# Kernel tuning notes

Measured on AMD Instinct MI355X. Metric: run time of the kernel, lower is better.

Reference implementation:

```python
import jax, jax.numpy as jnp
import numpy as np

N = 100000
E = 1600000
IN_C, HID_C, OUT_C = 128, 128, 64


def setup_inputs() -> dict:
    key = jax.random.key(0)
    k_x, k_e, k_w1, k_w2 = jax.random.split(key, 4)
    x = jax.random.normal(k_x, (N, IN_C), dtype=jnp.float32)
    edge_index = jax.random.randint(k_e, (2, E), 0, N, dtype=jnp.int32)
    # nn.Linear default init: U(-1/sqrt(fan_in), 1/sqrt(fan_in)); bias init zeros per module
    lim1 = 1.0 / np.sqrt(IN_C)
    lim2 = 1.0 / np.sqrt(HID_C)
    W1 = jax.random.uniform(k_w1, (IN_C, HID_C), minval=-lim1, maxval=lim1, dtype=jnp.float32)
    b1 = jnp.zeros((HID_C,), dtype=jnp.float32)
    W2 = jax.random.uniform(k_w2, (HID_C, OUT_C), minval=-lim2, maxval=lim2, dtype=jnp.float32)
    b2 = jnp.zeros((OUT_C,), dtype=jnp.float32)
    return {"x": x, "edge_index": edge_index, "W1": W1, "b1": b1, "W2": W2, "b2": b2}


def _out_degree_gcn_conv(x, src, dst, W, b, n_nodes):
    # linear projection (no bias in lin)
    h = x @ W  # [N, out_c]
    # out-degree of each source node
    deg = jax.ops.segment_sum(jnp.ones((src.shape[0],), dtype=h.dtype), src, num_segments=n_nodes)
    deg_inv = 1.0 / jnp.maximum(deg, 1.0)  # clamp(min=1)
    h = h * deg_inv[:, None]
    # message: x_j = h[src]; aggregate: sum at dst
    out = jax.ops.segment_sum(h[src], dst, num_segments=n_nodes)  # [N, out_c]
    return out + b


def reference(x, edge_index, W1, b1, W2, b2):
    src, dst = edge_index[0], edge_index[1]
    n = x.shape[0]
    h = _out_degree_gcn_conv(x, src, dst, W1, b1, n)
    h = jax.nn.relu(h)
    # dropout p=0.0 -> identity
    out = _out_degree_gcn_conv(h, src, dst, W2, b2, n)
    return out
```

## Files before the change

kernel.cpp:

```cpp
#include <hip/hip_runtime.h>
#include <hip/hip_bf16.h>


typedef __attribute__((ext_vector_type(8))) short short8;
typedef __attribute__((ext_vector_type(4))) float floatx4;

__device__ inline unsigned short f2bf(float f) {
    union { float f; unsigned u; } v; v.f = f;
    unsigned r = v.u + 0x7FFF + ((v.u >> 16) & 1);
    return (unsigned short)(r >> 16);
}
__device__ inline float bf2f(unsigned short b) {
    union { unsigned u; float f; } v; v.u = ((unsigned)b) << 16;
    return v.f;
}

#define NBMAX 512
#define CAP   8192

__global__ __launch_bounds__(256) void scatter2_kernel(
    const int* __restrict__ src, const int* __restrict__ dst, int E,
    int* __restrict__ cnt_d, int* __restrict__ cnt_s,
    unsigned* __restrict__ pairs, unsigned char* __restrict__ srcs_b, int NB)
{
    __shared__ int hd[NBMAX], bd[NBMAX], cd_[NBMAX];
    __shared__ int hs[NBMAX], bs[NBMAX], cs_[NBMAX];
    for (int i = threadIdx.x; i < NB; i += 256) { hd[i] = 0; cd_[i] = 0; hs[i] = 0; cs_[i] = 0; }
    __syncthreads();
    const int e0 = blockIdx.x * 8192;
    const int e1 = min(e0 + 8192, E);
    for (int i = e0 + threadIdx.x; i < e1; i += 256) {
        atomicAdd(&hd[dst[i] >> 8], 1);
        atomicAdd(&hs[src[i] >> 8], 1);
    }
    __syncthreads();
    for (int i = threadIdx.x; i < NB; i += 256) {
        if (hd[i]) bd[i] = atomicAdd(&cnt_d[i * 16], hd[i]);
        if (hs[i]) bs[i] = atomicAdd(&cnt_s[i * 16], hs[i]);
    }
    __syncthreads();
    for (int i = e0 + threadIdx.x; i < e1; i += 256) {
        int sv = src[i], dv = dst[i];
        int b = dv >> 8;
        int slot = atomicAdd(&cd_[b], 1);
        pairs[(size_t)b * CAP + bd[b] + slot] = ((unsigned)(dv & 255) << 24) | (unsigned)sv;
        int b2 = sv >> 8;
        int slot2 = atomicAdd(&cs_[b2], 1);
        srcs_b[(size_t)b2 * CAP + bs[b2] + slot2] = (unsigned char)(sv & 255);
    }
}

__global__ __launch_bounds__(256) void bucket_finalize_kernel(
    const unsigned* __restrict__ pairs, const unsigned char* __restrict__ srcs_b,
    const int* __restrict__ cnt_d, const int* __restrict__ cnt_s,
    int* __restrict__ sorted_src, int2* __restrict__ se,
    float* __restrict__ deg_inv, int N)
{
    const int b = blockIdx.x;
    const int node0 = b << 8;
    const int t = threadIdx.x;
    const size_t base = (size_t)b * CAP;
    __shared__ int hist[256];
    __shared__ int cur[256];
    __shared__ int pre[256];

    const int cd = cnt_d[b * 16];
    hist[t] = 0;
    __syncthreads();
    for (int i = t; i < cd; i += 256)
        atomicAdd(&hist[pairs[base + i] >> 24], 1);
    __syncthreads();
    int v = hist[t];
    pre[t] = v;
    __syncthreads();
    for (int o = 1; o < 256; o <<= 1) {
        int add = (t >= o) ? pre[t - o] : 0;
        __syncthreads();
        pre[t] += add;
        __syncthreads();
    }
    int excl = pre[t] - v;
    cur[t] = excl;
    if (node0 + t < N)
        se[node0 + t] = make_int2((int)base + excl, (int)base + excl + v);
    __syncthreads();
    for (int i = t; i < cd; i += 256) {
        unsigned p = pairs[base + i];
        int pos = atomicAdd(&cur[p >> 24], 1);
        sorted_src[base + pos] = (int)(p & 0xFFFFFFu);
    }

    __syncthreads();
    hist[t] = 0;
    __syncthreads();
    const int cs = cnt_s[b * 16];
    for (int i = t; i < cs; i += 256)
        atomicAdd(&hist[srcs_b[base + i]], 1);
    __syncthreads();
    if (node0 + t < N) {
        int d = hist[t];
        deg_inv[node0 + t] = 1.0f / (float)(d < 1 ? 1 : d);
    }
}

template <int NC, int AF>
__global__ __launch_bounds__(256) void gemm_mfma_kernel(
    const void* __restrict__ Ap, const float* __restrict__ W,
    const float* __restrict__ scale, unsigned short* __restrict__ Cb, int M)
{
    __shared__ unsigned short Al[64][136];
    __shared__ unsigned short Bl[NC][136];

    const int t = threadIdx.x;
    const int r0 = blockIdx.x * 64;

    for (int idx = t; idx < 64 * 32; idx += 256) {
        int r = idx >> 5, c4 = (idx & 31) << 2;
        int rg = r0 + r;
        ushort4 w;
        if (rg < M) {
            if (AF) {
                float s = scale[rg];
                float4 v = *(const float4*)&((const float*)Ap)[(size_t)rg * 128 + c4];
                w.x = f2bf(v.x * s); w.y = f2bf(v.y * s);
                w.z = f2bf(v.z * s); w.w = f2bf(v.w * s);
            } else {
                w = *(const ushort4*)&((const unsigned short*)Ap)[(size_t)rg * 128 + c4];
            }
        } else {
            w.x = w.y = w.z = w.w = 0;
        }
        *(ushort4*)&Al[r][c4] = w;
    }
    for (int idx = t; idx < 128 * (NC / 4); idx += 256) {
        int k = idx / (NC / 4), n4 = (idx % (NC / 4)) << 2;
        float4 v = *(const float4*)&W[(size_t)k * NC + n4];
        Bl[n4 + 0][k] = f2bf(v.x);
        Bl[n4 + 1][k] = f2bf(v.y);
        Bl[n4 + 2][k] = f2bf(v.z);
        Bl[n4 + 3][k] = f2bf(v.w);
    }
    __syncthreads();

    constexpr int NT = NC / 16;
    const int wm = t >> 6;
    const int lane = t & 63;
    const int lm = lane & 15;
    const int lk = (lane >> 4) * 8;

    floatx4 acc[NT];
#pragma unroll
    for (int j = 0; j < NT; ++j) acc[j] = (floatx4){0.f, 0.f, 0.f, 0.f};

#pragma unroll
    for (int kk = 0; kk < 4; ++kk) {
        const int kb = kk * 32 + lk;
        short8 af = *(const short8*)&Al[wm * 16 + lm][kb];
#pragma unroll
        for (int j = 0; j < NT; ++j) {
            short8 bfr = *(const short8*)&Bl[j * 16 + lm][kb];
            acc[j] = __builtin_amdgcn_mfma_f32_16x16x32_bf16(af, bfr, acc[j], 0, 0, 0);
        }
    }

    const int rbase = r0 + wm * 16 + (lane >> 4) * 4;
#pragma unroll
    for (int reg = 0; reg < 4; ++reg) {
        int rg = rbase + reg;
        if (rg < M) {
#pragma unroll
            for (int j = 0; j < NT; ++j)
                Cb[(size_t)rg * NC + j * 16 + lm] = f2bf(acc[j][reg]);
        }
    }
}

__global__ __launch_bounds__(256) void aggregate128_kernel(
    const int2* __restrict__ se, const int* __restrict__ sorted_src,
    const unsigned* __restrict__ val, const float* __restrict__ bias,
    const float* __restrict__ deg_inv, unsigned* __restrict__ outb, int N)
{
    int node = blockIdx.x * 8 + (threadIdx.x >> 5);
    if (node >= N) return;
    int l = threadIdx.x & 31;
    int2 r = se[node];
    int e = r.x;
    const int end = r.y;
    float a0 = 0.f, a1 = 0.f, a2 = 0.f, a3 = 0.f;
    for (; e + 4 <= end; e += 4) {
        int s0 = sorted_src[e + 0], s1 = sorted_src[e + 1];
        int s2 = sorted_src[e + 2], s3 = sorted_src[e + 3];
        uint2 v0 = *(const uint2*)&val[(size_t)s0 * 64 + 2 * l];
        uint2 v1 = *(const uint2*)&val[(size_t)s1 * 64 + 2 * l];
        uint2 v2 = *(const uint2*)&val[(size_t)s2 * 64 + 2 * l];
        uint2 v3 = *(const uint2*)&val[(size_t)s3 * 64 + 2 * l];
        a0 += (bf2f(v0.x & 0xFFFF) + bf2f(v1.x & 0xFFFF)) + (bf2f(v2.x & 0xFFFF) + bf2f(v3.x & 0xFFFF));
        a1 += (bf2f(v0.x >> 16) + bf2f(v1.x >> 16)) + (bf2f(v2.x >> 16) + bf2f(v3.x >> 16));
        a2 += (bf2f(v0.y & 0xFFFF) + bf2f(v1.y & 0xFFFF)) + (bf2f(v2.y & 0xFFFF) + bf2f(v3.y & 0xFFFF));
        a3 += (bf2f(v0.y >> 16) + bf2f(v1.y >> 16)) + (bf2f(v2.y >> 16) + bf2f(v3.y >> 16));
    }
    for (; e < end; ++e) {
        uint2 v = *(const uint2*)&val[(size_t)sorted_src[e] * 64 + 2 * l];
        a0 += bf2f(v.x & 0xFFFF);
        a1 += bf2f(v.x >> 16);
        a2 += bf2f(v.y & 0xFFFF);
        a3 += bf2f(v.y >> 16);
    }
    float di = deg_inv[node];
    float4 bv = *(const float4*)&bias[4 * l];
    a0 = fmaxf(a0 + bv.x, 0.f) * di;
    a1 = fmaxf(a1 + bv.y, 0.f) * di;
    a2 = fmaxf(a2 + bv.z, 0.f) * di;
    a3 = fmaxf(a3 + bv.w, 0.f) * di;
    uint2 o;
    o.x = (unsigned)f2bf(a0) | ((unsigned)f2bf(a1) << 16);
    o.y = (unsigned)f2bf(a2) | ((unsigned)f2bf(a3) << 16);
    *(uint2*)&outb[(size_t)node * 64 + 2 * l] = o;
}

__global__ __launch_bounds__(256) void aggregate64_kernel(
    const int2* __restrict__ se, const int* __restrict__ sorted_src,
    const unsigned* __restrict__ val, const float* __restrict__ bias,
    float* __restrict__ out, int N)
{
    int node = blockIdx.x * 8 + (threadIdx.x >> 5);
    if (node >= N) return;
    int l = threadIdx.x & 31;
    int2 r = se[node];
    int e = r.x;
    const int end = r.y;
    float ax = 0.f, ay = 0.f;
    for (; e + 4 <= end; e += 4) {
        int s0 = sorted_src[e + 0], s1 = sorted_src[e + 1];
        int s2 = sorted_src[e + 2], s3 = sorted_src[e + 3];
        unsigned v0 = val[(size_t)s0 * 32 + l];
        unsigned v1 = val[(size_t)s1 * 32 + l];
        unsigned v2 = val[(size_t)s2 * 32 + l];
        unsigned v3 = val[(size_t)s3 * 32 + l];
        ax += (bf2f(v0 & 0xFFFF) + bf2f(v1 & 0xFFFF)) + (bf2f(v2 & 0xFFFF) + bf2f(v3 & 0xFFFF));
        ay += (bf2f(v0 >> 16) + bf2f(v1 >> 16)) + (bf2f(v2 >> 16) + bf2f(v3 >> 16));
    }
    for (; e < end; ++e) {
        unsigned v = val[(size_t)sorted_src[e] * 32 + l];
        ax += bf2f(v & 0xFFFF);
        ay += bf2f(v >> 16);
    }
    float2 o = make_float2(ax + bias[2 * l], ay + bias[2 * l + 1]);
    *(float2*)&out[(size_t)node * 64 + 2 * l] = o;
}

extern "C" void kernel_launch(void* const* d_in, const int* in_sizes, int n_in,
                              void* d_out, int out_size, void* d_ws, size_t ws_size,
                              hipStream_t stream) {
    const float* x  = (const float*)d_in[0];
    const int*   ei = (const int*)d_in[1];
    const float* W1 = (const float*)d_in[2];
    const float* b1 = (const float*)d_in[3];
    const float* W2 = (const float*)d_in[4];
    const float* b2 = (const float*)d_in[5];
    float* out = (float*)d_out;

    const int N = in_sizes[0] / 128;
    const int E = in_sizes[1] / 2;
    const int* src = ei;
    const int* dst = ei + E;
    const int NB = (N + 255) >> 8;

    char* ws = (char*)d_ws;
    size_t off = 0;
    auto alloc = [&](size_t bytes) {
        void* p = ws + off;
        off = (off + bytes + 255) & ~(size_t)255;
        return p;
    };
    float* deg_inv  = (float*)alloc((size_t)N * 4);
    int2*  se       = (int2*)alloc((size_t)N * 8);
    int*   cnt_d    = (int*)alloc((size_t)NBMAX * 16 * 4 * 2);
    int*   cnt_s    = cnt_d + (size_t)NBMAX * 16;
    unsigned*      pairs  = (unsigned*)alloc((size_t)NBMAX * CAP * 4);
    unsigned char* srcs_b = (unsigned char*)alloc((size_t)NBMAX * CAP);
    int*   sorted_src = (int*)alloc((size_t)NBMAX * CAP * 4);
    unsigned short* h    = (unsigned short*)alloc((size_t)N * 128 * 2);
    unsigned short* out1 = (unsigned short*)alloc((size_t)N * 128 * 2);
    unsigned short* g    = h;

    hipMemsetAsync(cnt_d, 0, (size_t)NBMAX * 16 * 4 * 2, stream);

    scatter2_kernel<<<(E + 8191) / 8192, 256, 0, stream>>>(src, dst, E, cnt_d, cnt_s,
                                                           pairs, srcs_b, NB);
    bucket_finalize_kernel<<<NB, 256, 0, stream>>>(pairs, srcs_b, cnt_d, cnt_s,
                                                   sorted_src, se, deg_inv, N);

    const int gblocks = (N + 63) / 64;
    gemm_mfma_kernel<128, 1><<<gblocks, 256, 0, stream>>>(x, W1, deg_inv, h, N);
    aggregate128_kernel<<<(N + 7) / 8, 256, 0, stream>>>(se, sorted_src, (const unsigned*)h, b1,
                                                         deg_inv, (unsigned*)out1, N);
    gemm_mfma_kernel<64, 0><<<gblocks, 256, 0, stream>>>(out1, W2, deg_inv, g, N);
    aggregate64_kernel<<<(N + 7) / 8, 256, 0, stream>>>(se, sorted_src, (const unsigned*)g, b2, out, N);
}
```

Before: 319.4 us.

## Pre-convert weights to bf16, split aggregate channels, vectorize index loads

A new kernel converts W1 and W2 once into transposed bf16 buffers, and the GEMM reads B fragments straight from global memory instead of rebuilding a shared-memory copy in every block. The 128-channel aggregation is split into two channel-half blocks with interleaved block indexing, so each lane gathers 4 bytes per edge and there are more waves in flight. Edge segments are padded to multiples of 4 so neighbor indices can be loaded as aligned int4 with one-step prefetch, and the high-half bf16 unpack uses a mask instead of a shift. The trade-offs are that index reads are duplicated across the two channel halves and B fragments now come from global/L2 rather than LDS.

```diff
diff --git a/kernel.cpp b/kernel.cpp
--- a/kernel.cpp
+++ b/kernel.cpp
@@ -10,13 +10,33 @@
     unsigned r = v.u + 0x7FFF + ((v.u >> 16) & 1);
     return (unsigned short)(r >> 16);
 }
-__device__ inline float bf2f(unsigned short b) {
-    union { unsigned u; float f; } v; v.u = ((unsigned)b) << 16;
+__device__ inline float bf2f(unsigned b) {
+    union { unsigned u; float f; } v; v.u = b << 16;
+    return v.f;
+}
+__device__ inline float bf2f_hi(unsigned b) {
+    union { unsigned u; float f; } v; v.u = b & 0xFFFF0000u;
     return v.f;
 }
 
 #define NBMAX 512
 #define CAP   8192
+
+__global__ __launch_bounds__(256) void convw_kernel(
+    const float* __restrict__ W1, const float* __restrict__ W2,
+    unsigned short* __restrict__ Wb1, unsigned short* __restrict__ Wb2)
+{
+    int i = blockIdx.x * 256 + threadIdx.x;
+    if (i < 128 * 128) {
+        int k = i >> 7, n = i & 127;
+        Wb1[n * 128 + k] = f2bf(__builtin_bit_cast(unsigned, W1[k * 128 + n]) ? W1[k * 128 + n] : 0.0f);
+    }
+    i -= 128 * 128;
+    if (i >= 0 && i < 128 * 64) {
+        int k = i >> 6, n = i & 63;
+        Wb2[n * 128 + k] = f2bf(W2[k * 64 + n]);
+    }
+}
 
 __global__ __launch_bounds__(256) void scatter2_kernel(
     const int* __restrict__ src, const int* __restrict__ dst, int E,
@@ -71,7 +91,8 @@
         atomicAdd(&hist[pairs[base + i] >> 24], 1);
     __syncthreads();
     int v = hist[t];
-    pre[t] = v;
+    int v4 = (v + 3) & ~3;
+    pre[t] = v4;
     __syncthreads();
     for (int o = 1; o < 256; o <<= 1) {
         int add = (t >= o) ? pre[t - o] : 0;
@@ -79,7 +100,7 @@
         pre[t] += add;
         __syncthreads();
     }
-    int excl = pre[t] - v;
+    int excl = pre[t] - v4;
     cur[t] = excl;
     if (node0 + t < N)
         se[node0 + t] = make_int2((int)base + excl, (int)base + excl + v);
@@ -105,11 +126,10 @@
 
 template <int NC, int AF>
 __global__ __launch_bounds__(256) void gemm_mfma_kernel(
-    const void* __restrict__ Ap, const float* __restrict__ W,
+    const void* __restrict__ Ap, const unsigned short* __restrict__ Wb,
     const float* __restrict__ scale, unsigned short* __restrict__ Cb, int M)
 {
     __shared__ unsigned short Al[64][136];
-    __shared__ unsigned short Bl[NC][136];
 
     const int t = threadIdx.x;
     const int r0 = blockIdx.x * 64;
@@ -132,14 +152,6 @@
         }
         *(ushort4*)&Al[r][c4] = w;
     }
-    for (int idx = t; idx < 128 * (NC / 4); idx += 256) {
-        int k = idx / (NC / 4), n4 = (idx % (NC / 4)) << 2;
-        float4 v = *(const float4*)&W[(size_t)k * NC + n4];
-        Bl[n4 + 0][k] = f2bf(v.x);
-        Bl[n4 + 1][k] = f2bf(v.y);
-        Bl[n4 + 2][k] = f2bf(v.z);
-        Bl[n4 + 3][k] = f2bf(v.w);
-    }
     __syncthreads();
 
     constexpr int NT = NC / 16;
@@ -158,7 +170,7 @@
         short8 af = *(const short8*)&Al[wm * 16 + lm][kb];
 #pragma unroll
         for (int j = 0; j < NT; ++j) {
-            short8 bfr = *(const short8*)&Bl[j * 16 + lm][kb];
+            short8 bfr = *(const short8*)&Wb[(size_t)(j * 16 + lm) * 128 + kb];
             acc[j] = __builtin_amdgcn_mfma_f32_16x16x32_bf16(af, bfr, acc[j], 0, 0, 0);
         }
     }
@@ -180,42 +192,47 @@
     const unsigned* __restrict__ val, const float* __restrict__ bias,
     const float* __restrict__ deg_inv, unsigned* __restrict__ outb, int N)
 {
-    int node = blockIdx.x * 8 + (threadIdx.x >> 5);
+    const int blk = blockIdx.x;
+    const int u = (blk >> 3) * 4 + (blk & 3);
+    const int cg = (blk >> 2) & 1;
+    const int node = u * 8 + (threadIdx.x >> 5);
     if (node >= N) return;
-    int l = threadIdx.x & 31;
+    const int l = threadIdx.x & 31;
+    const int cbase = cg * 32 + l;
     int2 r = se[node];
     int e = r.x;
     const int end = r.y;
-    float a0 = 0.f, a1 = 0.f, a2 = 0.f, a3 = 0.f;
-    for (; e + 4 <= end; e += 4) {
-        int s0 = sorted_src[e + 0], s1 = sorted_src[e + 1];
-        int s2 = sorted_src[e + 2], s3 = sorted_src[e + 3];
-        uint2 v0 = *(const uint2*)&val[(size_t)s0 * 64 + 2 * l];
-        uint2 v1 = *(const uint2*)&val[(size_t)s1 * 64 + 2 * l];
-        uint2 v2 = *(const uint2*)&val[(size_t)s2 * 64 + 2 * l];
-        uint2 v3 = *(const uint2*)&val[(size_t)s3 * 64 + 2 * l];
-        a0 += (bf2f(v0.x & 0xFFFF) + bf2f(v1.x & 0xFFFF)) + (bf2f(v2.x & 0xFFFF) + bf2f(v3.x & 0xFFFF));
-        a1 += (bf2f(v0.x >> 16) + bf2f(v1.x >> 16)) + (bf2f(v2.x >> 16) + bf2f(v3.x >> 16));
-        a2 += (bf2f(v0.y & 0xFFFF) + bf2f(v1.y & 0xFFFF)) + (bf2f(v2.y & 0xFFFF) + bf2f(v3.y & 0xFFFF));
-        a3 += (bf2f(v0.y >> 16) + bf2f(v1.y >> 16)) + (bf2f(v2.y >> 16) + bf2f(v3.y >> 16));
+    float a0 = 0.f, a1 = 0.f;
+    if (e + 4 <= end) {
+        int4 idx = *(const int4*)&sorted_src[e];
+        for (; e + 8 <= end; e += 4) {
+            int4 nidx = *(const int4*)&sorted_src[e + 4];
+            unsigned v0 = val[(size_t)idx.x * 64 + cbase];
+            unsigned v1 = val[(size_t)idx.y * 64 + cbase];
+            unsigned v2 = val[(size_t)idx.z * 64 + cbase];
+            unsigned v3 = val[(size_t)idx.w * 64 + cbase];
+            a0 += (bf2f(v0 & 0xFFFF) + bf2f(v1 & 0xFFFF)) + (bf2f(v2 & 0xFFFF) + bf2f(v3 & 0xFFFF));
+            a1 += (bf2f_hi(v0) + bf2f_hi(v1)) + (bf2f_hi(v2) + bf2f_hi(v3));
+            idx = nidx;
+        }
+        unsigned v0 = val[(size_t)idx.x * 64 + cbase];
+        unsigned v1 = val[(size_t)idx.y * 64 + cbase];
+        unsigned v2 = val[(size_t)idx.z * 64 + cbase];
+        unsigned v3 = val[(size_t)idx.w * 64 + cbase];
+        a0 += (bf2f(v0 & 0xFFFF) + bf2f(v1 & 0xFFFF)) + (bf2f(v2 & 0xFFFF) + bf2f(v3 & 0xFFFF));
+        a1 += (bf2f_hi(v0) + bf2f_hi(v1)) + (bf2f_hi(v2) + bf2f_hi(v3));
+        e += 4;
     }
     for (; e < end; ++e) {
-        uint2 v = *(const uint2*)&val[(size_t)sorted_src[e] * 64 + 2 * l];
-        a0 += bf2f(v.x & 0xFFFF);
-        a1 += bf2f(v.x >> 16);
-        a2 += bf2f(v.y & 0xFFFF);
-        a3 += bf2f(v.y >> 16);
+        unsigned v = val[(size_t)sorted_src[e] * 64 + cbase];
+        a0 += bf2f(v & 0xFFFF);
+        a1 += bf2f_hi(v);
     }
     float di = deg_inv[node];
-    float4 bv = *(const float4*)&bias[4 * l];
+    float2 bv = *(const float2*)&bias[cg * 64 + 2 * l];
     a0 = fmaxf(a0 + bv.x, 0.f) * di;
     a1 = fmaxf(a1 + bv.y, 0.f) * di;
-    a2 = fmaxf(a2 + bv.z, 0.f) * di;
-    a3 = fmaxf(a3 + bv.w, 0.f) * di;
-    uint2 o;
-    o.x = (unsigned)f2bf(a0) | ((unsigned)f2bf(a1) << 16);
-    o.y = (unsigned)f2bf(a2) | ((unsigned)f2bf(a3) << 16);
-    *(uint2*)&outb[(size_t)node * 64 + 2 * l] = o;
+    outb[(size_t)node * 64 + cbase] = (unsigned)f2bf(a0) | ((unsigned)f2bf(a1) << 16);
 }
 
 __global__ __launch_bounds__(256) void aggregate64_kernel(
@@ -230,20 +247,30 @@
     int e = r.x;
     const int end = r.y;
     float ax = 0.f, ay = 0.f;
-    for (; e + 4 <= end; e += 4) {
-        int s0 = sorted_src[e + 0], s1 = sorted_src[e + 1];
-        int s2 = sorted_src[e + 2], s3 = sorted_src[e + 3];
-        unsigned v0 = val[(size_t)s0 * 32 + l];
-        unsigned v1 = val[(size_t)s1 * 32 + l];
-        unsigned v2 = val[(size_t)s2 * 32 + l];
-        unsigned v3 = val[(size_t)s3 * 32 + l];
+    if (e + 4 <= end) {
+        int4 idx = *(const int4*)&sorted_src[e];
+        for (; e + 8 <= end; e += 4) {
+            int4 nidx = *(const int4*)&sorted_src[e + 4];
+            unsigned v0 = val[(size_t)idx.x * 32 + l];
+            unsigned v1 = val[(size_t)idx.y * 32 + l];
+            unsigned v2 = val[(size_t)idx.z * 32 + l];
+            unsigned v3 = val[(size_t)idx.w * 32 + l];
+            ax += (bf2f(v0 & 0xFFFF) + bf2f(v1 & 0xFFFF)) + (bf2f(v2 & 0xFFFF) + bf2f(v3 & 0xFFFF));
+            ay += (bf2f_hi(v0) + bf2f_hi(v1)) + (bf2f_hi(v2) + bf2f_hi(v3));
+            idx = nidx;
+        }
+        unsigned v0 = val[(size_t)idx.x * 32 + l];
+        unsigned v1 = val[(size_t)idx.y * 32 + l];
+        unsigned v2 = val[(size_t)idx.z * 32 + l];
+        unsigned v3 = val[(size_t)idx.w * 32 + l];
         ax += (bf2f(v0 & 0xFFFF) + bf2f(v1 & 0xFFFF)) + (bf2f(v2 & 0xFFFF) + bf2f(v3 & 0xFFFF));
-        ay += (bf2f(v0 >> 16) + bf2f(v1 >> 16)) + (bf2f(v2 >> 16) + bf2f(v3 >> 16));
+        ay += (bf2f_hi(v0) + bf2f_hi(v1)) + (bf2f_hi(v2) + bf2f_hi(v3));
+        e += 4;
     }
     for (; e < end; ++e) {
         unsigned v = val[(size_t)sorted_src[e] * 32 + l];
         ax += bf2f(v & 0xFFFF);
-        ay += bf2f(v >> 16);
+        ay += bf2f_hi(v);
     }
     float2 o = make_float2(ax + bias[2 * l], ay + bias[2 * l + 1]);
     *(float2*)&out[(size_t)node * 64 + 2 * l] = o;
@@ -277,6 +304,8 @@
     int2*  se       = (int2*)alloc((size_t)N * 8);
     int*   cnt_d    = (int*)alloc((size_t)NBMAX * 16 * 4 * 2);
     int*   cnt_s    = cnt_d + (size_t)NBMAX * 16;
+    unsigned short* Wb1 = (unsigned short*)alloc((size_t)128 * 128 * 2);
+    unsigned short* Wb2 = (unsigned short*)alloc((size_t)64 * 128 * 2);
     unsigned*      pairs  = (unsigned*)alloc((size_t)NBMAX * CAP * 4);
     unsigned char* srcs_b = (unsigned char*)alloc((size_t)NBMAX * CAP);
     int*   sorted_src = (int*)alloc((size_t)NBMAX * CAP * 4);
@@ -286,15 +315,20 @@
 
     hipMemsetAsync(cnt_d, 0, (size_t)NBMAX * 16 * 4 * 2, stream);
 
+    convw_kernel<<<96, 256, 0, stream>>>(W1, W2, Wb1, Wb2);
     scatter2_kernel<<<(E + 8191) / 8192, 256, 0, stream>>>(src, dst, E, cnt_d, cnt_s,
                                                            pairs, srcs_b, NB);
     bucket_finalize_kernel<<<NB, 256, 0, stream>>>(pairs, srcs_b, cnt_d, cnt_s,
                                                    sorted_src, se, deg_inv, N);
 
     const int gblocks = (N + 63) / 64;
-    gemm_mfma_kernel<128, 1><<<gblocks, 256, 0, stream>>>(x, W1, deg_inv, h, N);
-    aggregate128_kernel<<<(N + 7) / 8, 256, 0, stream>>>(se, sorted_src, (const unsigned*)h, b1,
-                                                         deg_inv, (unsigned*)out1, N);
-    gemm_mfma_kernel<64, 0><<<gblocks, 256, 0, stream>>>(out1, W2, deg_inv, g, N);
+    gemm_mfma_kernel<128, 1><<<gblocks, 256, 0, stream>>>(x, Wb1, deg_inv, h, N);
+    {
+        const int G = (N + 7) / 8;
+        const int blocks = ((G + 3) / 4) * 8;
+        aggregate128_kernel<<<blocks, 256, 0, stream>>>(se, sorted_src, (const unsigned*)h, b1,
+                                                        deg_inv, (unsigned*)out1, N);
+    }
+    gemm_mfma_kernel<64, 0><<<gblocks, 256, 0, stream>>>(out1, Wb2, deg_inv, g, N);
     aggregate64_kernel<<<(N + 7) / 8, 256, 0, stream>>>(se, sorted_src, (const unsigned*)g, b2, out, N);
 }
```

New measurement: 330.1 us. 3.4% more time.
